# Performance work log

Measured on AMD Instinct MI355X. Metric: run time of the kernel, lower is better.

The kernel has to match this reference:

```python
import math
import jax, jax.numpy as jnp
import numpy as np

B, T, D, HS = 8, 2048, 1024, 64  # batch, seq (== block_size), d_embed, head_size
BLOCK_SIZE = 2048


def setup_inputs() -> dict:
    key = jax.random.key(0)
    kx, kq, kk, kv = jax.random.split(key, 4)
    x = jax.random.normal(kx, (B, T, D), dtype=jnp.float32)
    Wq = jax.random.normal(kq, (D, HS), dtype=jnp.float32) * (1.0 / math.sqrt(D))
    Wk = jax.random.normal(kk, (D, HS), dtype=jnp.float32) * (1.0 / math.sqrt(D))
    Wv = jax.random.normal(kv, (D, HS), dtype=jnp.float32) * (1.0 / math.sqrt(D))
    return {"x": x, "Wq": Wq, "Wk": Wk, "Wv": Wv}


def reference(x, Wq, Wk, Wv):
    # q, k, v: [B, T, HS]
    q = jnp.einsum("btd,dh->bth", x, Wq)
    k = jnp.einsum("btd,dh->bth", x, Wk)
    v = jnp.einsum("btd,dh->bth", x, Wv)
    # NOTE: original scales by 1/sqrt(block_size), not 1/sqrt(head_size)
    scale = 1.0 / math.sqrt(BLOCK_SIZE)
    scores = jnp.einsum("bqh,bkh->bqk", q, k) * scale  # [B, T, T]
    Tq = x.shape[1]
    causal = jnp.tril(jnp.ones((Tq, Tq), dtype=bool))
    scores = jnp.where(causal[None, :, :], scores, -jnp.inf)
    attn = jax.nn.softmax(scores, axis=-1)
    return jnp.einsum("bqk,bkh->bqh", attn, v)  # [B, T, HS]
```

## Files before the change

### kernel.cpp

```cpp
#include <hip/hip_runtime.h>

typedef unsigned short u16;
typedef unsigned int u32;
typedef float f32x4 __attribute__((ext_vector_type(4)));
typedef short s16x8 __attribute__((ext_vector_type(8)));

#define MFMA_BF16(a, b, c) __builtin_amdgcn_mfma_f32_16x16x32_bf16((a), (b), (c), 0, 0, 0)


__device__ __forceinline__ u16 f2bf(float f) {
  union { float f; u32 u; } v; v.f = f;
  u32 u = v.u;
  return (u16)((u + 0x7FFFu + ((u >> 16) & 1u)) >> 16);
}
__device__ __forceinline__ u16 f2bf_t(float f) {
  union { float f; u32 u; } v; v.f = f;
  return (u16)(v.u >> 16);
}
__device__ __forceinline__ s16x8 pack_bf8(float4 a, float4 b) {
  union { u32 d[4]; s16x8 v; } u;
  u.d[0] = (u32)f2bf(a.x) | ((u32)f2bf(a.y) << 16);
  u.d[1] = (u32)f2bf(a.z) | ((u32)f2bf(a.w) << 16);
  u.d[2] = (u32)f2bf(b.x) | ((u32)f2bf(b.y) << 16);
  u.d[3] = (u32)f2bf(b.z) | ((u32)f2bf(b.w) << 16);
  return u.v;
}

__global__ __launch_bounds__(256) void wt_convert(const float* __restrict__ Wq,
                                                  const float* __restrict__ Wk,
                                                  const float* __restrict__ Wv,
                                                  u16* __restrict__ Wt2) {
  __shared__ u16 Ls[64][70];
  const int bid = blockIdx.x;
  const int m = bid >> 4, d0 = (bid & 15) * 64;
  const float* W = (m == 0) ? Wq : (m == 1) ? Wk : Wv;
  const int t = threadIdx.x;
  {
    const int dr = t >> 2, hc = (t & 3) * 16;
    const float4* src = (const float4*)(W + (size_t)(d0 + dr) * 64 + hc);
    float4 f0 = src[0], f1 = src[1], f2 = src[2], f3 = src[3];
    float fl[16] = {f0.x, f0.y, f0.z, f0.w, f1.x, f1.y, f1.z, f1.w,
                    f2.x, f2.y, f2.z, f2.w, f3.x, f3.y, f3.z, f3.w};
#pragma unroll
    for (int j = 0; j < 8; ++j) {
      u32 pk = (u32)f2bf(fl[2 * j]) | ((u32)f2bf(fl[2 * j + 1]) << 16);
      *(u32*)&Ls[dr][hc + 2 * j] = pk;
    }
  }
  __syncthreads();
  {
    const int h = t >> 2, dcs = (t & 3) * 16;
    const int row = m * 64 + h;
    u32 po[8];
#pragma unroll
    for (int j = 0; j < 8; ++j)
      po[j] = (u32)Ls[dcs + 2 * j][h] | ((u32)Ls[dcs + 2 * j + 1][h] << 16);
    const int kg0 = (d0 + dcs) >> 3;
    *(uint4*)&Wt2[((size_t)kg0 * 192 + row) * 8] = make_uint4(po[0], po[1], po[2], po[3]);
    *(uint4*)&Wt2[((size_t)(kg0 + 1) * 192 + row) * 8] = make_uint4(po[4], po[5], po[6], po[7]);
  }
}

__global__ __launch_bounds__(256) void qkv_gemm(const float* __restrict__ x,
                                                const u16* __restrict__ Wt2,
                                                u16* __restrict__ qo,
                                                u16* __restrict__ ko,
                                                u16* __restrict__ vTo) {
  __shared__ float M[3][16][196];
  const int tid = threadIdx.x, lane = tid & 63, w = tid >> 6;
  const int lc = lane & 15, hi = lane >> 4;
  const int m0 = blockIdx.x * 16;

  f32x4 acc[12];
#pragma unroll
  for (int i = 0; i < 12; ++i) acc[i] = (f32x4){0.f, 0.f, 0.f, 0.f};

  const float* xp = x + (size_t)(m0 + lc) * 1024 + w * 256 + hi * 8;
  const u16* wp = Wt2 + (size_t)(w * 32 + hi) * 1536 + lc * 8;

  for (int t = 0; t < 8; ++t) {
    float4 xa = *(const float4*)(xp + t * 32);
    float4 xb = *(const float4*)(xp + t * 32 + 4);
    s16x8 aq = pack_bf8(xa, xb);
    const u16* wk = wp + (size_t)t * 4 * 1536;
#pragma unroll
    for (int j = 0; j < 12; ++j) {
      s16x8 bf = *(const s16x8*)(wk + j * 128);
      acc[j] = MFMA_BF16(aq, bf, acc[j]);
    }
  }

  if (w > 0) {
#pragma unroll
    for (int j = 0; j < 12; ++j)
#pragma unroll
      for (int r = 0; r < 4; ++r) M[w - 1][hi * 4 + r][j * 16 + lc] = acc[j][r];
  }
  __syncthreads();
  if (w == 0) {
#pragma unroll
    for (int j = 0; j < 12; ++j) {
#pragma unroll
      for (int r = 0; r < 4; ++r) {
        const int row = hi * 4 + r, n = j * 16 + lc;
        float val = acc[j][r] + M[0][row][n] + M[1][row][n] + M[2][row][n];
        u16 bvv = f2bf(val);
        const int gr = m0 + row;
        if (j < 4) {
          qo[gr * 64 + n] = bvv;
        } else if (j < 8) {
          ko[gr * 64 + (n - 64)] = bvv;
        } else {
          int b = gr >> 11, t2 = gr & 2047;
          vTo[((b << 6) + (n - 128)) * 2048 + t2] = bvv;
        }
      }
    }
  }
}

__global__ __launch_bounds__(256, 2) void attn_fwd(const u16* __restrict__ qb,
                                                   const u16* __restrict__ kb,
                                                   const u16* __restrict__ vT,
                                                   float* __restrict__ out) {
  __shared__ float PoS[4][32][66];
  __shared__ float Pl[4][32];
  const int tid = threadIdx.x, lane = tid & 63, w = tid >> 6;
  const int lc = lane & 15, hi = lane >> 4;
  const int bid = blockIdx.x;
  const int b = bid & 7, v = 63 - (bid >> 3);
  const int q0 = v * 32;
  const int brow = b * 2048;
  u16* Pw = (u16*)&PoS[w][0][0];

  s16x8 aq[2][2];
#pragma unroll
  for (int sub = 0; sub < 2; ++sub) {
    const u16* qrow = qb + (size_t)(brow + q0 + sub * 16 + lc) * 64;
    aq[sub][0] = *(const s16x8*)(qrow + hi * 8);
    aq[sub][1] = *(const s16x8*)(qrow + 32 + hi * 8);
  }

  f32x4 o[2][4];
  float lrow[2][4];
#pragma unroll
  for (int sub = 0; sub < 2; ++sub)
#pragma unroll
    for (int i = 0; i < 4; ++i) {
      o[sub][i] = (f32x4){0.f, 0.f, 0.f, 0.f};
      lrow[sub][i] = 0.f;
    }

  const float SL = 0.031879357f;
  const int nk = v + 1;
  const int c = (nk + 3) >> 2;
  const int s = w;
  const int it0 = s * c;
  const int it1 = min(it0 + c, nk);

  const u16* kbase = kb + (size_t)brow * 64;

  for (int it = it0; it < it1; ++it) {
    const int kvb = it * 32;
    const u16* krow0 = kbase + (size_t)(kvb + lc) * 64;
    const u16* krow1 = kbase + (size_t)(kvb + 16 + lc) * 64;
    s16x8 k00 = *(const s16x8*)(krow0 + hi * 8);
    s16x8 k01 = *(const s16x8*)(krow0 + 32 + hi * 8);
    s16x8 k10 = *(const s16x8*)(krow1 + hi * 8);
    s16x8 k11 = *(const s16x8*)(krow1 + 32 + hi * 8);
    s16x8 bv[4];
#pragma unroll
    for (int nt = 0; nt < 4; ++nt)
      bv[nt] = *(const s16x8*)&vT[(size_t)(b * 64 + nt * 16 + lc) * 2048 + kvb + hi * 8];

    f32x4 sc[2][2];
#pragma unroll
    for (int sub = 0; sub < 2; ++sub) {
      sc[sub][0] = (f32x4){0.f, 0.f, 0.f, 0.f};
      sc[sub][1] = (f32x4){0.f, 0.f, 0.f, 0.f};
      sc[sub][0] = MFMA_BF16(aq[sub][0], k00, sc[sub][0]);
      sc[sub][0] = MFMA_BF16(aq[sub][1], k01, sc[sub][0]);
      sc[sub][1] = MFMA_BF16(aq[sub][0], k10, sc[sub][1]);
      sc[sub][1] = MFMA_BF16(aq[sub][1], k11, sc[sub][1]);
    }

    if (kvb + 31 <= q0) {
#pragma unroll
      for (int sub = 0; sub < 2; ++sub)
#pragma unroll
        for (int r = 0; r < 4; ++r) {
          float p0 = exp2f(sc[sub][0][r] * SL);
          float p1 = exp2f(sc[sub][1][r] * SL);
          lrow[sub][r] += p0 + p1;
          Pw[(sub * 16 + hi * 4 + r) * 40 + lc] = f2bf_t(p0);
          Pw[(sub * 16 + hi * 4 + r) * 40 + 16 + lc] = f2bf_t(p1);
        }
    } else {
#pragma unroll
      for (int sub = 0; sub < 2; ++sub)
#pragma unroll
        for (int r = 0; r < 4; ++r) {
          const int qt = q0 + sub * 16 + hi * 4 + r;
          const int kv0 = kvb + lc;
          float p0 = (kv0 <= qt) ? exp2f(sc[sub][0][r] * SL) : 0.f;
          float p1 = (kv0 + 16 <= qt) ? exp2f(sc[sub][1][r] * SL) : 0.f;
          lrow[sub][r] += p0 + p1;
          Pw[(sub * 16 + hi * 4 + r) * 40 + lc] = f2bf_t(p0);
          Pw[(sub * 16 + hi * 4 + r) * 40 + 16 + lc] = f2bf_t(p1);
        }
    }
    asm volatile("s_waitcnt lgkmcnt(0)" ::: "memory");
    s16x8 pa0 = *(const s16x8*)&Pw[lc * 40 + hi * 8];
    s16x8 pa1 = *(const s16x8*)&Pw[(16 + lc) * 40 + hi * 8];
#pragma unroll
    for (int nt = 0; nt < 4; ++nt) {
      o[0][nt] = MFMA_BF16(pa0, bv[nt], o[0][nt]);
      o[1][nt] = MFMA_BF16(pa1, bv[nt], o[1][nt]);
    }
  }

#pragma unroll
  for (int sub = 0; sub < 2; ++sub)
#pragma unroll
    for (int r = 0; r < 4; ++r) {
      float l = lrow[sub][r];
      l += __shfl_xor(l, 1);
      l += __shfl_xor(l, 2);
      l += __shfl_xor(l, 4);
      l += __shfl_xor(l, 8);
      lrow[sub][r] = l;
    }

  if (lc == 0) {
#pragma unroll
    for (int sub = 0; sub < 2; ++sub)
#pragma unroll
      for (int r = 0; r < 4; ++r) Pl[w][sub * 16 + hi * 4 + r] = lrow[sub][r];
  }
  float* Pow = &PoS[w][0][0];
#pragma unroll
  for (int sub = 0; sub < 2; ++sub)
#pragma unroll
    for (int nt = 0; nt < 4; ++nt)
#pragma unroll
      for (int r = 0; r < 4; ++r)
        Pow[(sub * 16 + hi * 4 + r) * 66 + nt * 16 + lc] = o[sub][nt][r];
  __syncthreads();

#pragma unroll
  for (int rr = 0; rr < 8; ++rr) {
    const int row = w * 8 + rr;
    float L = Pl[0][row] + Pl[1][row] + Pl[2][row] + Pl[3][row];
    float val = PoS[0][row][lane] + PoS[1][row][lane] + PoS[2][row][lane] + PoS[3][row][lane];
    out[(size_t)(brow + q0 + row) * 64 + lane] = val / L;
  }
}

extern "C" void kernel_launch(void* const* d_in, const int* in_sizes, int n_in,
                              void* d_out, int out_size, void* d_ws, size_t ws_size,
                              hipStream_t stream) {
  (void)in_sizes; (void)n_in; (void)out_size; (void)ws_size;
  const float* x = (const float*)d_in[0];
  const float* Wq = (const float*)d_in[1];
  const float* Wk = (const float*)d_in[2];
  const float* Wv = (const float*)d_in[3];
  float* out = (float*)d_out;

  u16* wsu = (u16*)d_ws;
  u16* Wt = wsu;
  u16* qb = Wt + 192 * 1024;
  u16* kb = qb + 8 * 2048 * 64;
  u16* vT = kb + 8 * 2048 * 64;

  wt_convert<<<48, 256, 0, stream>>>(Wq, Wk, Wv, Wt);
  qkv_gemm<<<1024, 256, 0, stream>>>(x, Wt, qb, kb, vT);
  attn_fwd<<<512, 256, 0, stream>>>(qb, kb, vT, out);
}
```

Measured before the change: 62.38 us.

## Stage QKV weights in LDS with double-buffered async loads in projection GEMM

The QKV projection GEMM is restructured so each 512-thread block handles 32 rows and stages swizzled bf16 weight tiles into LDS through global_load_lds, double-buffered across 16 k-steps. Converted x tiles also go through LDS, and each wave computes a 2x3 MFMA tile with a two-way split-K reduction. Before, every wave read weight fragments straight from global memory and did a four-way split-K. The aim is more weight reuse per block and load latency hidden behind MFMA work, at the cost of more LDS and a barrier on every k-step.

```diff
diff --git a/kernel.cpp b/kernel.cpp
--- a/kernel.cpp
+++ b/kernel.cpp
@@ -25,14 +25,18 @@
   u.d[3] = (u32)f2bf(b.z) | ((u32)f2bf(b.w) << 16);
   return u.v;
 }
+__device__ __forceinline__ void gload_lds16(const u16* g, u16* l) {
+  __builtin_amdgcn_global_load_lds((const __attribute__((address_space(1))) u32*)(const void*)g,
+                                   (__attribute__((address_space(3))) u32*)(void*)l, 16, 0, 0);
+}
 
 __global__ __launch_bounds__(256) void wt_convert(const float* __restrict__ Wq,
                                                   const float* __restrict__ Wk,
                                                   const float* __restrict__ Wv,
-                                                  u16* __restrict__ Wt2) {
+                                                  u16* __restrict__ Wt3) {
   __shared__ u16 Ls[64][70];
   const int bid = blockIdx.x;
-  const int m = bid >> 4, d0 = (bid & 15) * 64;
+  const int m = bid >> 4, kstep = bid & 15, d0 = kstep * 64;
   const float* W = (m == 0) ? Wq : (m == 1) ? Wk : Wv;
   const int t = threadIdx.x;
   {
@@ -50,72 +54,125 @@
   __syncthreads();
   {
     const int h = t >> 2, dcs = (t & 3) * 16;
-    const int row = m * 64 + h;
+    const int grow = m * 64 + h;
     u32 po[8];
 #pragma unroll
     for (int j = 0; j < 8; ++j)
       po[j] = (u32)Ls[dcs + 2 * j][h] | ((u32)Ls[dcs + 2 * j + 1][h] << 16);
-    const int kg0 = (d0 + dcs) >> 3;
-    *(uint4*)&Wt2[((size_t)kg0 * 192 + row) * 8] = make_uint4(po[0], po[1], po[2], po[3]);
-    *(uint4*)&Wt2[((size_t)(kg0 + 1) * 192 + row) * 8] = make_uint4(po[4], po[5], po[6], po[7]);
-  }
-}
-
-__global__ __launch_bounds__(256) void qkv_gemm(const float* __restrict__ x,
-                                                const u16* __restrict__ Wt2,
+    u16* dst = Wt3 + (size_t)kstep * 12288 + grow * 64 + dcs;
+    *(uint4*)&dst[0] = make_uint4(po[0], po[1], po[2], po[3]);
+    *(uint4*)&dst[8] = make_uint4(po[4], po[5], po[6], po[7]);
+  }
+}
+
+__global__ __launch_bounds__(512) void qkv_gemm(const float* __restrict__ x,
+                                                const u16* __restrict__ Wt3,
                                                 u16* __restrict__ qo,
                                                 u16* __restrict__ ko,
                                                 u16* __restrict__ vTo) {
-  __shared__ float M[3][16][196];
+  __shared__ u16 Wl[2][12288];
+  __shared__ u16 Xs[2][2048];
   const int tid = threadIdx.x, lane = tid & 63, w = tid >> 6;
   const int lc = lane & 15, hi = lane >> 4;
-  const int m0 = blockIdx.x * 16;
-
-  f32x4 acc[12];
-#pragma unroll
-  for (int i = 0; i < 12; ++i) acc[i] = (f32x4){0.f, 0.f, 0.f, 0.f};
-
-  const float* xp = x + (size_t)(m0 + lc) * 1024 + w * 256 + hi * 8;
-  const u16* wp = Wt2 + (size_t)(w * 32 + hi) * 1536 + lc * 8;
-
-  for (int t = 0; t < 8; ++t) {
-    float4 xa = *(const float4*)(xp + t * 32);
-    float4 xb = *(const float4*)(xp + t * 32 + 4);
-    s16x8 aq = pack_bf8(xa, xb);
-    const u16* wk = wp + (size_t)t * 4 * 1536;
-#pragma unroll
-    for (int j = 0; j < 12; ++j) {
-      s16x8 bf = *(const s16x8*)(wk + j * 128);
-      acc[j] = MFMA_BF16(aq, bf, acc[j]);
-    }
-  }
-
-  if (w > 0) {
-#pragma unroll
-    for (int j = 0; j < 12; ++j)
-#pragma unroll
-      for (int r = 0; r < 4; ++r) M[w - 1][hi * 4 + r][j * 16 + lc] = acc[j][r];
-  }
-  __syncthreads();
-  if (w == 0) {
-#pragma unroll
-    for (int j = 0; j < 12; ++j) {
-#pragma unroll
-      for (int r = 0; r < 4; ++r) {
-        const int row = hi * 4 + r, n = j * 16 + lc;
-        float val = acc[j][r] + M[0][row][n] + M[1][row][n] + M[2][row][n];
-        u16 bvv = f2bf(val);
-        const int gr = m0 + row;
-        if (j < 4) {
-          qo[gr * 64 + n] = bvv;
-        } else if (j < 8) {
-          ko[gr * 64 + (n - 64)] = bvv;
-        } else {
-          int b = gr >> 11, t2 = gr & 2047;
-          vTo[((b << 6) + (n - 128)) * 2048 + t2] = bvv;
+  const int m0 = blockIdx.x * 32;
+  const int ntg = w & 3, ksub = w >> 2;
+
+  f32x4 acc[2][3];
+#pragma unroll
+  for (int a = 0; a < 2; ++a)
+#pragma unroll
+    for (int i = 0; i < 3; ++i) acc[a][i] = (f32x4){0.f, 0.f, 0.f, 0.f};
+
+  const int wr_r = (lane >> 3);
+  const int wr_g = (lane & 7) ^ ((lane >> 3) & 7);
+  const int xrow = tid >> 3, xsg = tid & 7;
+  const int xg = xsg ^ (xrow & 7);
+  const float* xptr = x + (size_t)(m0 + xrow) * 1024 + xsg * 8;
+
+  const int ga = ((ksub * 4 + hi) ^ (lc & 7)) * 8;
+
+  auto stage_w = [&](int t, int buf) {
+#pragma unroll
+    for (int c = 0; c < 3; ++c) {
+      const int i = w * 3 + c;
+      const int r = i * 8 + wr_r;
+      gload_lds16(Wt3 + (size_t)t * 12288 + r * 64 + wr_g * 8, &Wl[buf][i * 512]);
+    }
+  };
+
+  {
+    stage_w(0, 0);
+    if (tid < 256) {
+      float4 xa = *(const float4*)xptr;
+      float4 xb = *(const float4*)(xptr + 4);
+      s16x8 p = pack_bf8(xa, xb);
+      *(s16x8*)&Xs[0][xrow * 64 + xg * 8] = p;
+    }
+  }
+  __syncthreads();
+  int buf = 0;
+
+  for (int t = 0; t < 16; ++t) {
+    float4 xa, xb;
+    if (t < 15) {
+      xa = *(const float4*)(xptr + (t + 1) * 64);
+      xb = *(const float4*)(xptr + (t + 1) * 64 + 4);
+      stage_w(t + 1, buf ^ 1);
+    }
+    s16x8 a0 = *(const s16x8*)&Xs[buf][(0 * 16 + lc) * 64 + ga];
+    s16x8 a1 = *(const s16x8*)&Xs[buf][(1 * 16 + lc) * 64 + ga];
+#pragma unroll
+    for (int j = 0; j < 3; ++j) {
+      const int row = (ntg * 3 + j) * 16 + lc;
+      s16x8 bfr = *(const s16x8*)&Wl[buf][row * 64 + ga];
+      acc[0][j] = MFMA_BF16(a0, bfr, acc[0][j]);
+      acc[1][j] = MFMA_BF16(a1, bfr, acc[1][j]);
+    }
+    if (t < 15) {
+      if (tid < 256) {
+        s16x8 p = pack_bf8(xa, xb);
+        *(s16x8*)&Xs[buf ^ 1][xrow * 64 + xg * 8] = p;
+      }
+      __syncthreads();
+      buf ^= 1;
+    }
+  }
+
+  float* M = (float*)&Wl[0][0];
+  __syncthreads();
+  if (ksub == 1) {
+#pragma unroll
+    for (int ms = 0; ms < 2; ++ms)
+#pragma unroll
+      for (int j = 0; j < 3; ++j)
+#pragma unroll
+        for (int r = 0; r < 4; ++r)
+          M[ntg * 1536 + (ms * 16 + hi * 4 + r) * 48 + j * 16 + lc] = acc[ms][j][r];
+  }
+  __syncthreads();
+  if (ksub == 0) {
+#pragma unroll
+    for (int ms = 0; ms < 2; ++ms)
+#pragma unroll
+      for (int j = 0; j < 3; ++j) {
+        const int nt = ntg * 3 + j;
+#pragma unroll
+        for (int r = 0; r < 4; ++r) {
+          const int row = ms * 16 + hi * 4 + r;
+          float val = acc[ms][j][r] + M[ntg * 1536 + row * 48 + j * 16 + lc];
+          u16 bvv = f2bf(val);
+          const int gr = m0 + row;
+          const int n = nt * 16 + lc;
+          if (nt < 4) {
+            qo[gr * 64 + n] = bvv;
+          } else if (nt < 8) {
+            ko[gr * 64 + (n - 64)] = bvv;
+          } else {
+            int b = gr >> 11, t2 = gr & 2047;
+            vTo[((b << 6) + (n - 128)) * 2048 + t2] = bvv;
+          }
         }
       }
-    }
   }
 }
 
@@ -273,6 +330,6 @@
   u16* vT = kb + 8 * 2048 * 64;
 
   wt_convert<<<48, 256, 0, stream>>>(Wq, Wk, Wv, Wt);
-  qkv_gemm<<<1024, 256, 0, stream>>>(x, Wt, qb, kb, vT);
+  qkv_gemm<<<512, 512, 0, stream>>>(x, Wt, qb, kb, vT);
   attn_fwd<<<512, 256, 0, stream>>>(qb, kb, vT, out);
 }
```

Measured after the change: 56.98 us. 8.7% less time.

## Restructure QKV GEMM into LDS-tiled, double-buffered blocks with async global-to-LDS loads

Applied to the files above, without the earlier changes.

The QKV projection kernel now processes 64 rows per 1024-thread block, staging x and the weight tiles into LDS through global_load_lds with XOR swizzling and double buffering across 16 k-steps. Each wave computes a 16x48 output slice, which removes the split-K reduction through shared memory. The weight conversion kernel writes a per-k-step row-major layout to match the staging. Weights are now reused from LDS across 64 rows instead of being reloaded per 16-row block. The trade-off is fewer blocks (256) and higher LDS use per block.

```diff
diff --git a/kernel.cpp b/kernel.cpp
--- a/kernel.cpp
+++ b/kernel.cpp
@@ -25,14 +25,18 @@
   u.d[3] = (u32)f2bf(b.z) | ((u32)f2bf(b.w) << 16);
   return u.v;
 }
+__device__ __forceinline__ void gload_lds16(const void* g, void* l) {
+  __builtin_amdgcn_global_load_lds((const __attribute__((address_space(1))) u32*)g,
+                                   (__attribute__((address_space(3))) u32*)l, 16, 0, 0);
+}
 
 __global__ __launch_bounds__(256) void wt_convert(const float* __restrict__ Wq,
                                                   const float* __restrict__ Wk,
                                                   const float* __restrict__ Wv,
-                                                  u16* __restrict__ Wt2) {
+                                                  u16* __restrict__ Wt3) {
   __shared__ u16 Ls[64][70];
   const int bid = blockIdx.x;
-  const int m = bid >> 4, d0 = (bid & 15) * 64;
+  const int m = bid >> 4, kstep = bid & 15, d0 = kstep * 64;
   const float* W = (m == 0) ? Wq : (m == 1) ? Wk : Wv;
   const int t = threadIdx.x;
   {
@@ -50,70 +54,88 @@
   __syncthreads();
   {
     const int h = t >> 2, dcs = (t & 3) * 16;
-    const int row = m * 64 + h;
+    const int grow = m * 64 + h;
     u32 po[8];
 #pragma unroll
     for (int j = 0; j < 8; ++j)
       po[j] = (u32)Ls[dcs + 2 * j][h] | ((u32)Ls[dcs + 2 * j + 1][h] << 16);
-    const int kg0 = (d0 + dcs) >> 3;
-    *(uint4*)&Wt2[((size_t)kg0 * 192 + row) * 8] = make_uint4(po[0], po[1], po[2], po[3]);
-    *(uint4*)&Wt2[((size_t)(kg0 + 1) * 192 + row) * 8] = make_uint4(po[4], po[5], po[6], po[7]);
-  }
-}
-
-__global__ __launch_bounds__(256) void qkv_gemm(const float* __restrict__ x,
-                                                const u16* __restrict__ Wt2,
-                                                u16* __restrict__ qo,
-                                                u16* __restrict__ ko,
-                                                u16* __restrict__ vTo) {
-  __shared__ float M[3][16][196];
+    u16* dst = Wt3 + (size_t)kstep * 12288 + grow * 64 + dcs;
+    *(uint4*)&dst[0] = make_uint4(po[0], po[1], po[2], po[3]);
+    *(uint4*)&dst[8] = make_uint4(po[4], po[5], po[6], po[7]);
+  }
+}
+
+__global__ __launch_bounds__(1024) void qkv_gemm(const float* __restrict__ x,
+                                                 const u16* __restrict__ Wt3,
+                                                 u16* __restrict__ qo,
+                                                 u16* __restrict__ ko,
+                                                 u16* __restrict__ vTo) {
+  __shared__ float Xf[2][4096];
+  __shared__ u16 Wl[2][12288];
   const int tid = threadIdx.x, lane = tid & 63, w = tid >> 6;
   const int lc = lane & 15, hi = lane >> 4;
-  const int m0 = blockIdx.x * 16;
-
-  f32x4 acc[12];
-#pragma unroll
-  for (int i = 0; i < 12; ++i) acc[i] = (f32x4){0.f, 0.f, 0.f, 0.f};
-
-  const float* xp = x + (size_t)(m0 + lc) * 1024 + w * 256 + hi * 8;
-  const u16* wp = Wt2 + (size_t)(w * 32 + hi) * 1536 + lc * 8;
-
-  for (int t = 0; t < 8; ++t) {
-    float4 xa = *(const float4*)(xp + t * 32);
-    float4 xb = *(const float4*)(xp + t * 32 + 4);
-    s16x8 aq = pack_bf8(xa, xb);
-    const u16* wk = wp + (size_t)t * 4 * 1536;
-#pragma unroll
-    for (int j = 0; j < 12; ++j) {
-      s16x8 bf = *(const s16x8*)(wk + j * 128);
-      acc[j] = MFMA_BF16(aq, bf, acc[j]);
-    }
-  }
-
-  if (w > 0) {
-#pragma unroll
-    for (int j = 0; j < 12; ++j)
-#pragma unroll
-      for (int r = 0; r < 4; ++r) M[w - 1][hi * 4 + r][j * 16 + lc] = acc[j][r];
-  }
+  const int m0 = blockIdx.x * 64;
+  const int msub = w & 3, ntg = w >> 2;
+
+  f32x4 acc[3];
+#pragma unroll
+  for (int i = 0; i < 3; ++i) acc[i] = (f32x4){0.f, 0.f, 0.f, 0.f};
+
+  const int rX = w * 4 + (lane >> 4);
+  const int gX = (lane & 15) ^ (rX & 15);
+  const float* xsrc = x + (size_t)(m0 + rX) * 1024 + gX * 4;
+  const int rW = w * 8 + (lane >> 3);
+  const int gW = (lane & 7) ^ (rW & 7);
+  const u16* wsrc = Wt3 + rW * 64 + gW * 8;
+
+  auto stage = [&](int t, int bf) {
+    gload_lds16(xsrc + t * 64, &Xf[bf][w * 256]);
+    gload_lds16(wsrc + (size_t)t * 12288, &Wl[bf][w * 512]);
+    if (w < 8) gload_lds16(wsrc + (size_t)t * 12288 + 8192, &Wl[bf][(16 + w) * 512]);
+  };
+
+  stage(0, 0);
   __syncthreads();
-  if (w == 0) {
-#pragma unroll
-    for (int j = 0; j < 12; ++j) {
-#pragma unroll
-      for (int r = 0; r < 4; ++r) {
-        const int row = hi * 4 + r, n = j * 16 + lc;
-        float val = acc[j][r] + M[0][row][n] + M[1][row][n] + M[2][row][n];
-        u16 bvv = f2bf(val);
-        const int gr = m0 + row;
-        if (j < 4) {
-          qo[gr * 64 + n] = bvv;
-        } else if (j < 8) {
-          ko[gr * 64 + (n - 64)] = bvv;
-        } else {
-          int b = gr >> 11, t2 = gr & 2047;
-          vTo[((b << 6) + (n - 128)) * 2048 + t2] = bvv;
-        }
+  int buf = 0;
+
+  const int rA = msub * 16 + lc;
+  for (int t = 0; t < 16; ++t) {
+    if (t < 15) stage(t + 1, buf ^ 1);
+#pragma unroll
+    for (int ksub = 0; ksub < 2; ++ksub) {
+      const int g0 = ksub * 8 + hi * 2;
+      float4 alo = *(const float4*)&Xf[buf][rA * 64 + ((g0 ^ (rA & 15)) << 2)];
+      float4 ahi = *(const float4*)&Xf[buf][rA * 64 + (((g0 + 1) ^ (rA & 15)) << 2)];
+      s16x8 a = pack_bf8(alo, ahi);
+#pragma unroll
+      for (int j = 0; j < 3; ++j) {
+        const int rB = (ntg * 3 + j) * 16 + lc;
+        const int gB = (ksub * 4 + hi) ^ (rB & 7);
+        s16x8 b = *(const s16x8*)&Wl[buf][rB * 64 + gB * 8];
+        acc[j] = MFMA_BF16(a, b, acc[j]);
+      }
+    }
+    if (t < 15) {
+      __syncthreads();
+      buf ^= 1;
+    }
+  }
+
+#pragma unroll
+  for (int j = 0; j < 3; ++j) {
+    const int nt = ntg * 3 + j;
+#pragma unroll
+    for (int r = 0; r < 4; ++r) {
+      const int gr = m0 + msub * 16 + hi * 4 + r;
+      const u16 val = f2bf(acc[j][r]);
+      const int n = nt * 16 + lc;
+      if (nt < 4) {
+        qo[gr * 64 + n] = val;
+      } else if (nt < 8) {
+        ko[gr * 64 + (n - 64)] = val;
+      } else {
+        int b = gr >> 11, t2 = gr & 2047;
+        vTo[((b << 6) + (n - 128)) * 2048 + t2] = val;
       }
     }
   }
@@ -273,6 +295,6 @@
   u16* vT = kb + 8 * 2048 * 64;
 
   wt_convert<<<48, 256, 0, stream>>>(Wq, Wk, Wv, Wt);
-  qkv_gemm<<<1024, 256, 0, stream>>>(x, Wt, qb, kb, vT);
+  qkv_gemm<<<256, 1024, 0, stream>>>(x, Wt, qb, kb, vT);
   attn_fwd<<<512, 256, 0, stream>>>(qb, kb, vT, out);
 }
```

After: 58.80 us. -5.7%, faster.

## Restructure QKV GEMM to split N across waves with register prefetch, no LDS reduction

Applied to the files above, without the earlier changes.

The QKV projection kernel now gives each of 8 waves a 16-row by 48-column output tile over the full K=1024, instead of splitting K across 4 waves and reducing partial sums through shared memory. It software-prefetches the next x and weight fragments in registers and uses the HIP bf16 pair-conversion intrinsic for packing. This removes the LDS reduction and barrier and lets more waves work at once. In exchange each wave runs a longer serial K loop, and x rows are reloaded by the four waves that share them.

```diff
diff --git a/kernel.cpp b/kernel.cpp
--- a/kernel.cpp
+++ b/kernel.cpp
@@ -1,4 +1,5 @@
 #include <hip/hip_runtime.h>
+#include <hip/hip_bf16.h>
 
 typedef unsigned short u16;
 typedef unsigned int u32;
@@ -18,12 +19,12 @@
   return (u16)(v.u >> 16);
 }
 __device__ __forceinline__ s16x8 pack_bf8(float4 a, float4 b) {
-  union { u32 d[4]; s16x8 v; } u;
-  u.d[0] = (u32)f2bf(a.x) | ((u32)f2bf(a.y) << 16);
-  u.d[1] = (u32)f2bf(a.z) | ((u32)f2bf(a.w) << 16);
-  u.d[2] = (u32)f2bf(b.x) | ((u32)f2bf(b.y) << 16);
-  u.d[3] = (u32)f2bf(b.z) | ((u32)f2bf(b.w) << 16);
-  return u.v;
+  union { __hip_bfloat162 h2[4]; s16x8 s; } u;
+  u.h2[0] = __float22bfloat162_rn(make_float2(a.x, a.y));
+  u.h2[1] = __float22bfloat162_rn(make_float2(a.z, a.w));
+  u.h2[2] = __float22bfloat162_rn(make_float2(b.x, b.y));
+  u.h2[3] = __float22bfloat162_rn(make_float2(b.z, b.w));
+  return u.s;
 }
 
 __global__ __launch_bounds__(256) void wt_convert(const float* __restrict__ Wq,
@@ -61,59 +62,61 @@
   }
 }
 
-__global__ __launch_bounds__(256) void qkv_gemm(const float* __restrict__ x,
+__global__ __launch_bounds__(512) void qkv_gemm(const float* __restrict__ x,
                                                 const u16* __restrict__ Wt2,
                                                 u16* __restrict__ qo,
                                                 u16* __restrict__ ko,
                                                 u16* __restrict__ vTo) {
-  __shared__ float M[3][16][196];
   const int tid = threadIdx.x, lane = tid & 63, w = tid >> 6;
   const int lc = lane & 15, hi = lane >> 4;
-  const int m0 = blockIdx.x * 16;
-
-  f32x4 acc[12];
-#pragma unroll
-  for (int i = 0; i < 12; ++i) acc[i] = (f32x4){0.f, 0.f, 0.f, 0.f};
-
-  const float* xp = x + (size_t)(m0 + lc) * 1024 + w * 256 + hi * 8;
-  const u16* wp = Wt2 + (size_t)(w * 32 + hi) * 1536 + lc * 8;
-
-  for (int t = 0; t < 8; ++t) {
-    float4 xa = *(const float4*)(xp + t * 32);
-    float4 xb = *(const float4*)(xp + t * 32 + 4);
-    s16x8 aq = pack_bf8(xa, xb);
-    const u16* wk = wp + (size_t)t * 4 * 1536;
-#pragma unroll
-    for (int j = 0; j < 12; ++j) {
-      s16x8 bf = *(const s16x8*)(wk + j * 128);
-      acc[j] = MFMA_BF16(aq, bf, acc[j]);
-    }
-  }
-
-  if (w > 0) {
-#pragma unroll
-    for (int j = 0; j < 12; ++j)
-#pragma unroll
-      for (int r = 0; r < 4; ++r) M[w - 1][hi * 4 + r][j * 16 + lc] = acc[j][r];
-  }
-  __syncthreads();
-  if (w == 0) {
-#pragma unroll
-    for (int j = 0; j < 12; ++j) {
-#pragma unroll
-      for (int r = 0; r < 4; ++r) {
-        const int row = hi * 4 + r, n = j * 16 + lc;
-        float val = acc[j][r] + M[0][row][n] + M[1][row][n] + M[2][row][n];
-        u16 bvv = f2bf(val);
-        const int gr = m0 + row;
-        if (j < 4) {
-          qo[gr * 64 + n] = bvv;
-        } else if (j < 8) {
-          ko[gr * 64 + (n - 64)] = bvv;
-        } else {
-          int b = gr >> 11, t2 = gr & 2047;
-          vTo[((b << 6) + (n - 128)) * 2048 + t2] = bvv;
-        }
+  const int m0 = blockIdx.x * 32;
+  const int msub = w & 1, ntg = w >> 1;
+
+  f32x4 acc[3];
+#pragma unroll
+  for (int i = 0; i < 3; ++i) acc[i] = (f32x4){0.f, 0.f, 0.f, 0.f};
+
+  const float4* xp = (const float4*)(x + (size_t)(m0 + msub * 16 + lc) * 1024 + hi * 8);
+  const u16* wp = Wt2 + ((size_t)hi * 192 + ntg * 48 + lc) * 8;
+
+  float4 xa = xp[0], xb = xp[1];
+  s16x8 b0 = *(const s16x8*)(wp);
+  s16x8 b1 = *(const s16x8*)(wp + 128);
+  s16x8 b2 = *(const s16x8*)(wp + 256);
+
+  for (int kk = 0; kk < 32; ++kk) {
+    float4 na, nb;
+    s16x8 n0, n1, n2;
+    if (kk < 31) {
+      na = xp[kk * 8 + 8];
+      nb = xp[kk * 8 + 9];
+      const u16* wn = wp + (size_t)(kk + 1) * 6144;
+      n0 = *(const s16x8*)(wn);
+      n1 = *(const s16x8*)(wn + 128);
+      n2 = *(const s16x8*)(wn + 256);
+    }
+    s16x8 a = pack_bf8(xa, xb);
+    acc[0] = MFMA_BF16(a, b0, acc[0]);
+    acc[1] = MFMA_BF16(a, b1, acc[1]);
+    acc[2] = MFMA_BF16(a, b2, acc[2]);
+    if (kk < 31) { xa = na; xb = nb; b0 = n0; b1 = n1; b2 = n2; }
+  }
+
+#pragma unroll
+  for (int j = 0; j < 3; ++j) {
+    const int nt = ntg * 3 + j;
+#pragma unroll
+    for (int r = 0; r < 4; ++r) {
+      const int gr = m0 + msub * 16 + hi * 4 + r;
+      const u16 val = f2bf(acc[j][r]);
+      const int n = nt * 16 + lc;
+      if (nt < 4) {
+        qo[gr * 64 + n] = val;
+      } else if (nt < 8) {
+        ko[gr * 64 + (n - 64)] = val;
+      } else {
+        int b = gr >> 11, t2 = gr & 2047;
+        vTo[((b << 6) + (n - 128)) * 2048 + t2] = val;
       }
     }
   }
@@ -273,6 +276,6 @@
   u16* vT = kb + 8 * 2048 * 64;
 
   wt_convert<<<48, 256, 0, stream>>>(Wq, Wk, Wv, Wt);
-  qkv_gemm<<<1024, 256, 0, stream>>>(x, Wt, qb, kb, vT);
+  qkv_gemm<<<512, 512, 0, stream>>>(x, Wt, qb, kb, vT);
   attn_fwd<<<512, 256, 0, stream>>>(qb, kb, vT, out);
 }
```

Result: slower. 78.19 us (+25.3%).
